# Kernel tuning notes

Hardware: AMD Instinct MI355X
Metric: run time of the kernel (lower is better)

## Reference

```python
import jax, jax.numpy as jnp
import numpy as np
import math

NUM_HEADS = 16
NUM_KV_HEADS = 4
HEAD_DIM = 128
ROPE_THETA = 10000.0


def _rope(x, cos, sin):
    # x: [b, h, s, d]; cos/sin: [1, 1, s, d//2]
    half = x.shape[-1] // 2
    x1, x2 = x[..., :half], x[..., half:]
    return jnp.concatenate([x1 * cos - x2 * sin, x2 * cos + x1 * sin], axis=-1)


def setup_inputs() -> dict:
    key = jax.random.key(0)
    ks = jax.random.split(key, 5)
    B, S, H = 2, 2048, 2048
    scale_qk = (2.0 / (H + H)) ** 0.5
    scale_kv = (2.0 / (H + NUM_KV_HEADS * HEAD_DIM)) ** 0.5
    return {
        "hidden_states": jax.random.normal(ks[0], (B, S, H), jnp.float32),
        "Wq": jax.random.normal(ks[1], (NUM_HEADS * HEAD_DIM, H), jnp.float32) * scale_qk,
        "Wk": jax.random.normal(ks[2], (NUM_KV_HEADS * HEAD_DIM, H), jnp.float32) * scale_kv,
        "Wv": jax.random.normal(ks[3], (NUM_KV_HEADS * HEAD_DIM, H), jnp.float32) * scale_kv,
        "Wo": jax.random.normal(ks[4], (NUM_HEADS * HEAD_DIM, H), jnp.float32) * scale_qk,
    }


def reference(hidden_states, Wq, Wk, Wv, Wo):
    B, S, H = hidden_states.shape
    hd = HEAD_DIM

    q = (hidden_states @ Wq.T).reshape(B, S, NUM_HEADS, hd).transpose(0, 2, 1, 3)
    k = (hidden_states @ Wk.T).reshape(B, S, NUM_KV_HEADS, hd).transpose(0, 2, 1, 3)
    v = (hidden_states @ Wv.T).reshape(B, S, NUM_KV_HEADS, hd).transpose(0, 2, 1, 3)

    # RoPE (half-split variant, as in module)
    inv_freq = 1.0 / (ROPE_THETA ** (jnp.arange(0, hd, 2, dtype=jnp.float32) / hd))
    pos = jnp.arange(S, dtype=jnp.float32)
    freqs = pos[:, None] * inv_freq[None, :]           # [S, hd//2]
    cos = jnp.cos(freqs)[None, None]                   # [1,1,S,hd//2]
    sin = jnp.sin(freqs)[None, None]
    q = _rope(q, cos, sin)
    k = _rope(k, cos, sin)

    # GQA: repeat kv heads (repeat_interleave semantics)
    n_rep = NUM_HEADS // NUM_KV_HEADS
    k = jnp.repeat(k, n_rep, axis=1)
    v = jnp.repeat(v, n_rep, axis=1)

    scores = jnp.einsum("bhqd,bhkd->bhqk", q, k) / math.sqrt(hd)
    attn = jax.nn.softmax(scores, axis=-1)
    out = jnp.einsum("bhqk,bhkd->bhqd", attn, v)
    out = out.transpose(0, 2, 1, 3).reshape(B, S, NUM_HEADS * hd)
    return out @ Wo.T
```

## Files before the change

### kernel.cpp

```cpp
#include <hip/hip_runtime.h>
#include <cstdint>
#include <cstddef>

typedef __bf16 bf16x8 __attribute__((ext_vector_type(8)));
typedef __bf16 bf16x4 __attribute__((ext_vector_type(4)));
typedef float  f32x4  __attribute__((ext_vector_type(4)));

__device__ __forceinline__ void gload_lds16(const void* g, void* l) {
    __builtin_amdgcn_global_load_lds(
        (const __attribute__((address_space(1))) void*)g,
        (__attribute__((address_space(3))) void*)l, 16, 0, 0);
}

#define VM6B asm volatile("s_waitcnt vmcnt(6) lgkmcnt(0)\ns_barrier" ::: "memory")
#define VM4B asm volatile("s_waitcnt vmcnt(4) lgkmcnt(0)\ns_barrier" ::: "memory")
#define VM0B asm volatile("s_waitcnt vmcnt(0) lgkmcnt(0)\ns_barrier" ::: "memory")
#define BARO asm volatile("s_barrier" ::: "memory")
#define WAITB4 asm volatile("s_waitcnt vmcnt(4) lgkmcnt(0)\ns_barrier" ::: "memory")
#define WAITB0 asm volatile("s_waitcnt vmcnt(0) lgkmcnt(0)\ns_barrier" ::: "memory")

#define SEQ 2048
#define NH 16
#define NKV 4
#define HD 128

__global__ __launch_bounds__(256) void cvt_all(const float* __restrict__ hs,
                                               const float* __restrict__ wq,
                                               const float* __restrict__ wk,
                                               const float* __restrict__ wv,
                                               const float* __restrict__ wo,
                                               __bf16* __restrict__ hB,
                                               __bf16* __restrict__ WqkB,
                                               __bf16* __restrict__ WvB,
                                               __bf16* __restrict__ WoB) {
    for (int bid = blockIdx.x; bid < 18432; bid += gridDim.x) {
        const float* in; __bf16* out; int base;
        if (bid < 8192)        { in = hs; out = hB;                   base = bid; }
        else if (bid < 12288)  { in = wq; out = WqkB;                 base = bid - 8192; }
        else if (bid < 13312)  { in = wk; out = WqkB + 2048 * 2048;   base = bid - 12288; }
        else if (bid < 14336)  { in = wv; out = WvB;                  base = bid - 13312; }
        else                   { in = wo; out = WoB;                  base = bid - 14336; }
        int i = base * 256 + threadIdx.x;
        float4 v = ((const float4*)in)[i];
        bf16x4 o = { (__bf16)v.x, (__bf16)v.y, (__bf16)v.z, (__bf16)v.w };
        ((bf16x4*)out)[i] = o;
    }
}

__device__ __forceinline__ void stage_half(const __bf16* __restrict__ M,
                                           char* dbuf, int bmn, int k0, int half,
                                           int wave, int lane) {
    char* hb = dbuf + (half & 1) * 32768 + (half >> 1) * 16384;
    int kbase = k0 + (half >> 1) * 32;
#pragma unroll
    for (int g = 0; g < 2; ++g) {
        int c = wave * 2 + g;
        int row = (c & 3) * 64 + lane;
        int ks = c >> 2;
        gload_lds16(M + (size_t)(bmn + row) * 2048 + kbase + ks * 8, hb + c * 1024);
    }
}

template <int KS, int MH>
__device__ __forceinline__ void phase_mfma(const __bf16* bA, const __bf16* bB,
                                           int quad, int l16, int wr128, int colbase,
                                           bf16x8 (&bq)[4], f32x4 acc[8][4]) {
    bf16x8 af[4];
#pragma unroll
    for (int ii = 0; ii < 4; ++ii)
        af[ii] = *(const bf16x8*)(bA + (KS * 4 + quad) * 2048 +
                                  (wr128 + (MH * 4 + ii) * 16 + l16) * 8);
    if (MH == 0) {
#pragma unroll
        for (int j = 0; j < 4; ++j)
            bq[j] = *(const bf16x8*)(bB + (KS * 4 + quad) * 2048 +
                                     (colbase + (j & 1) * 16 + (j >> 1) * 64 + l16) * 8);
    }
    __builtin_amdgcn_s_setprio(1);
#pragma unroll
    for (int ii = 0; ii < 4; ++ii)
#pragma unroll
        for (int j = 0; j < 4; ++j)
            acc[MH * 4 + ii][j] = __builtin_amdgcn_mfma_f32_16x16x32_bf16(
                af[ii], bq[j], acc[MH * 4 + ii][j], 0, 0, 0);
    __builtin_amdgcn_s_setprio(0);
}

__device__ __forceinline__ void gemm_core(const __bf16* __restrict__ A,
                                          const __bf16* __restrict__ B,
                                          char* lds, int bm, int bn,
                                          int wave, int lane, int quad, int l16,
                                          int wr128, int colbase, f32x4 acc[8][4]) {
    const int NT = 32;
    stage_half(A, lds, bm, 0, 0, wave, lane);
    stage_half(B, lds, bn, 0, 1, wave, lane);
    stage_half(A, lds, bm, 0, 2, wave, lane);
    stage_half(B, lds, bn, 0, 3, wave, lane);
    int cur = 0;
    for (int t = 0; t < NT - 1; ++t) {
        const __bf16* bA = (const __bf16*)(lds + cur * 65536);
        const __bf16* bB = (const __bf16*)(lds + cur * 65536 + 32768);
        char* nb = lds + (cur ^ 1) * 65536;
        int k1 = (t + 1) * 64;
        bf16x8 bq[4];
        stage_half(A, nb, bm, k1, 0, wave, lane);
        VM6B;
        phase_mfma<0, 0>(bA, bB, quad, l16, wr128, colbase, bq, acc);
        stage_half(B, nb, bn, k1, 1, wave, lane);
        BARO;
        phase_mfma<0, 1>(bA, bB, quad, l16, wr128, colbase, bq, acc);
        stage_half(A, nb, bm, k1, 2, wave, lane);
        VM6B;
        phase_mfma<1, 0>(bA, bB, quad, l16, wr128, colbase, bq, acc);
        stage_half(B, nb, bn, k1, 3, wave, lane);
        BARO;
        phase_mfma<1, 1>(bA, bB, quad, l16, wr128, colbase, bq, acc);
        cur ^= 1;
    }
    {
        const __bf16* bA = (const __bf16*)(lds + cur * 65536);
        const __bf16* bB = (const __bf16*)(lds + cur * 65536 + 32768);
        bf16x8 bq[4];
        VM4B;
        phase_mfma<0, 0>(bA, bB, quad, l16, wr128, colbase, bq, acc);
        phase_mfma<0, 1>(bA, bB, quad, l16, wr128, colbase, bq, acc);
        VM0B;
        phase_mfma<1, 0>(bA, bB, quad, l16, wr128, colbase, bq, acc);
        phase_mfma<1, 1>(bA, bB, quad, l16, wr128, colbase, bq, acc);
    }
}

__global__ __launch_bounds__(512, 2) void qkv_gemm(const __bf16* __restrict__ hB,
                                                   const __bf16* __restrict__ Wqk,
                                                   const __bf16* __restrict__ Wv,
                                                   __bf16* __restrict__ Qr,
                                                   __bf16* __restrict__ Kr,
                                                   __bf16* __restrict__ VT) {
    __shared__ __align__(16) char lds[2 * 65536];
    const int tid = threadIdx.x;
    const int wave = tid >> 6, lane = tid & 63;
    const int quad = lane >> 4, l16 = lane & 15;
    const int wr = wave >> 2, wc = wave & 3;
    int wg = blockIdx.y * 16 + blockIdx.x;
    wg = (wg & 7) * 24 + (wg >> 3);
    const int x = wg & 15, y = wg >> 4;
    const bool isVT = (y >= 10);
    const bool isQ = (y < 8);

    const __bf16* Amat = isVT ? Wv : hB;
    const __bf16* Bmat = isVT ? hB : (isQ ? Wqk : Wqk + 2048 * 2048);
    const int bm = isVT ? (y - 10) * 256 : x * 256;
    const int bn = isVT ? x * 256 : (isQ ? y * 256 : (y - 8) * 256);

    const int wr128 = wr * 128;
    const int colbase = (wc >> 1) * 128 + (wc & 1) * 32;

    f32x4 acc[8][4] = {};
    gemm_core(Amat, Bmat, lds, bm, bn, wave, lane, quad, l16, wr128, colbase, acc);

    if (isVT) {
#pragma unroll
        for (int i = 0; i < 8; ++i)
#pragma unroll
            for (int j = 0; j < 4; ++j) {
                int row = bm + wr128 + i * 16 + quad * 4;
                int col = bn + colbase + (j & 1) * 16 + (j >> 1) * 64 + l16;
#pragma unroll
                for (int r = 0; r < 4; ++r)
                    VT[(size_t)(row + r) * 4096 + col] = (__bf16)acc[i][j][r];
            }
    } else {
        __bf16* outp = isQ ? Qr : Kr;
        const float sc = isQ ? 0.1275255128608411f : 1.0f;
        const int nh = isQ ? NH : NKV;
        const int hh = (isQ ? y * 2 : (y - 8) * 2) + (wc >> 1);
#pragma unroll
        for (int j2 = 0; j2 < 2; ++j2) {
            int d = (wc & 1) * 32 + j2 * 16 + l16;
            float inv = exp2f(-(float)d * 0.2076205059304601f);
#pragma unroll
            for (int i = 0; i < 8; ++i)
#pragma unroll
                for (int r = 0; r < 4; ++r) {
                    int m = bm + wr128 + i * 16 + quad * 4 + r;
                    int s = m & (SEQ - 1), b = m >> 11;
                    float f = (float)s * inv;
                    float c = __cosf(f) * sc, sn = __sinf(f) * sc;
                    float x1 = acc[i][j2][r], x2 = acc[i][j2 + 2][r];
                    size_t rb = ((size_t)(b * nh + hh) * SEQ + s) * HD;
                    outp[rb + d]      = (__bf16)(x1 * c - x2 * sn);
                    outp[rb + d + 64] = (__bf16)(x2 * c + x1 * sn);
                }
        }
    }
}

__global__ __launch_bounds__(512, 1) void gemm_bt_f32(const __bf16* __restrict__ A,
                                                      const __bf16* __restrict__ W,
                                                      float* __restrict__ C) {
    __shared__ __align__(16) char lds[3 * 49152];
    const int tid = threadIdx.x;
    const int wave = tid >> 6, lane = tid & 63;
    const int quad = lane >> 4, l16 = lane & 15;
    const int wr = wave >> 2, wc = wave & 3;
    int wg = blockIdx.y * 32 + blockIdx.x;
    wg = (wg & 7) * 32 + (wg >> 3);
    const int bm = (wg & 31) * 128, bn = (wg >> 5) * 256;

    f32x4 acc[4][4] = {};

    auto stageT = [&](int sb, int k0) {
        char* dst = lds + sb * 49152;
#pragma unroll
        for (int tt = 0; tt < 6; ++tt) {
            int c = wave * 6 + tt;
            if (c < 16) {
                int row = ((c & 1) << 6) + lane;
                gload_lds16(A + (size_t)(bm + row) * 2048 + k0 + (c >> 1) * 8,
                            dst + c * 1024);
            } else {
                int vc = c - 16;
                int row = ((vc & 3) << 6) + lane;
                gload_lds16(W + (size_t)(bn + row) * 2048 + k0 + (vc >> 2) * 8,
                            dst + 16384 + vc * 1024);
            }
        }
    };

    auto computeT = [&](int cb2) {
        const __bf16* bA = (const __bf16*)(lds + cb2 * 49152);
        const __bf16* bB = bA + 8192;
#pragma unroll
        for (int ks = 0; ks < 2; ++ks) {
            bf16x8 af[4], bq[4];
#pragma unroll
            for (int i = 0; i < 4; ++i)
                af[i] = *(const bf16x8*)(bA + (ks * 4 + quad) * 1024 +
                                         (wr * 64 + i * 16 + l16) * 8);
#pragma unroll
            for (int j = 0; j < 4; ++j)
                bq[j] = *(const bf16x8*)(bB + (ks * 4 + quad) * 2048 +
                                         (wc * 64 + j * 16 + l16) * 8);
            __builtin_amdgcn_s_setprio(1);
#pragma unroll
            for (int i = 0; i < 4; ++i)
#pragma unroll
                for (int j = 0; j < 4; ++j)
                    acc[i][j] = __builtin_amdgcn_mfma_f32_16x16x32_bf16(
                        af[i], bq[j], acc[i][j], 0, 0, 0);
            __builtin_amdgcn_s_setprio(0);
        }
    };

    stageT(0, 0);
    stageT(1, 64);
    int cb = 0;
    for (int t = 0; t < 31; ++t) {
        VM6B;
        if (t < 30) {
            int sb = cb + 2; if (sb >= 3) sb -= 3;
            stageT(sb, (t + 2) * 64);
        }
        computeT(cb);
        if (++cb == 3) cb = 0;
    }
    VM0B;
    computeT(cb);

#pragma unroll
    for (int i = 0; i < 4; ++i)
#pragma unroll
        for (int j = 0; j < 4; ++j) {
            int row = bm + wr * 64 + i * 16 + quad * 4;
            int col = bn + wc * 64 + j * 16 + l16;
#pragma unroll
            for (int r = 0; r < 4; ++r)
                C[(size_t)(row + r) * 2048 + col] = acc[i][j][r];
        }
}

__global__ __launch_bounds__(256, 2) void attn_kernel(const __bf16* __restrict__ Q,
                                                      const __bf16* __restrict__ Kr,
                                                      const __bf16* __restrict__ VT,
                                                      __bf16* __restrict__ AO) {
    __shared__ __align__(16) char ring[3 * 16384];
    __shared__ __align__(16) __bf16 Pb[4][32][40];

    const int tid = threadIdx.x;
    const int wave = tid >> 6, lane = tid & 63;
    const int quad = lane >> 4, l16 = lane & 15;
    int wg = (blockIdx.z * 16 + blockIdx.y) * 16 + blockIdx.x;
    wg = (wg & 7) * 64 + (wg >> 3);
    const int x = wg & 15, h = (wg >> 4) & 15, b = wg >> 8;
    const int kv = h >> 2;
    const int qbase = x * 128 + wave * 32;

    bf16x8 qf[2][4];
#pragma unroll
    for (int qs = 0; qs < 2; ++qs) {
        const __bf16* Qp =
            Q + ((size_t)(b * NH + h) * SEQ + qbase + qs * 16 + l16) * HD + quad * 8;
#pragma unroll
        for (int kq = 0; kq < 4; ++kq) qf[qs][kq] = *(const bf16x8*)(Qp + kq * 32);
    }

    const __bf16* Kp = Kr + (size_t)(b * NKV + kv) * SEQ * HD;
    const __bf16* Vp = VT + (size_t)(kv * HD) * (2 * SEQ) + b * SEQ;

    f32x4 oacc[2][8] = {};
    float lpart[2] = {0.f, 0.f};

    auto stage = [&](int sb, int k0) {
        char* dst = ring + sb * 16384;
#pragma unroll
        for (int tt = 0; tt < 4; ++tt) {
            int c = wave * 4 + tt;
            if (c < 8) {
                gload_lds16(Kp + (size_t)(k0 + (lane & 31)) * HD +
                                (2 * c + (lane >> 5)) * 8,
                            dst + c * 1024);
            } else {
                int vc = c - 8;
                gload_lds16(Vp + (size_t)(((vc & 1) << 6) + lane) * (2 * SEQ) + k0 +
                                (vc >> 1) * 8,
                            dst + 8192 + vc * 1024);
            }
        }
    };

    auto compute = [&](int cb) {
        const __bf16* kt = (const __bf16*)(ring + cb * 16384);
        const __bf16* vt = kt + 4096;
#pragma unroll
        for (int mt = 0; mt < 2; ++mt) {
            f32x4 s0 = {0.f, 0.f, 0.f, 0.f}, s1 = {0.f, 0.f, 0.f, 0.f};
#pragma unroll
            for (int kq = 0; kq < 4; ++kq) {
                bf16x8 ka = *(const bf16x8*)(kt + (kq * 4 + quad) * 256 +
                                             (mt * 16 + l16) * 8);
                s0 = __builtin_amdgcn_mfma_f32_16x16x32_bf16(ka, qf[0][kq], s0, 0, 0, 0);
                s1 = __builtin_amdgcn_mfma_f32_16x16x32_bf16(ka, qf[1][kq], s1, 0, 0, 0);
            }
            bf16x4 pk0, pk1;
#pragma unroll
            for (int r = 0; r < 4; ++r) {
                float p0 = __builtin_amdgcn_exp2f(s0[r]);
                float p1 = __builtin_amdgcn_exp2f(s1[r]);
                lpart[0] += p0; lpart[1] += p1;
                pk0[r] = (__bf16)p0; pk1[r] = (__bf16)p1;
            }
            *(bf16x4*)&Pb[wave][l16][mt * 16 + quad * 4] = pk0;
            *(bf16x4*)&Pb[wave][16 + l16][mt * 16 + quad * 4] = pk1;
        }
        bf16x8 pb0 = *(const bf16x8*)&Pb[wave][l16][quad * 8];
        bf16x8 pb1 = *(const bf16x8*)&Pb[wave][16 + l16][quad * 8];
#pragma unroll
        for (int mt = 0; mt < 8; ++mt) {
            bf16x8 va = *(const bf16x8*)(vt + quad * 1024 + (mt * 16 + l16) * 8);
            oacc[0][mt] = __builtin_amdgcn_mfma_f32_16x16x32_bf16(
                va, pb0, oacc[0][mt], 0, 0, 0);
            oacc[1][mt] = __builtin_amdgcn_mfma_f32_16x16x32_bf16(
                va, pb1, oacc[1][mt], 0, 0, 0);
        }
    };

    stage(0, 0);
    stage(1, 32);
    int cb = 0;
    for (int t = 0; t < 63; ++t) {
        WAITB4;
        if (t < 62) {
            int sb = cb + 2; if (sb >= 3) sb -= 3;
            stage(sb, (t + 2) * 32);
        }
        compute(cb);
        if (++cb == 3) cb = 0;
    }
    WAITB0;
    compute(cb);

#pragma unroll
    for (int qs = 0; qs < 2; ++qs) {
        lpart[qs] += __shfl_xor(lpart[qs], 16);
        lpart[qs] += __shfl_xor(lpart[qs], 32);
        float inv = 1.f / lpart[qs];
        int q = qbase + qs * 16 + l16;
#pragma unroll
        for (int mt = 0; mt < 8; ++mt) {
            bf16x4 ov;
#pragma unroll
            for (int r = 0; r < 4; ++r) ov[r] = (__bf16)(oacc[qs][mt][r] * inv);
            *(bf16x4*)(AO + ((size_t)(b * SEQ + q)) * (NH * HD) + h * HD +
                       mt * 16 + quad * 4) = ov;
        }
    }
}

extern "C" void kernel_launch(void* const* d_in, const int* in_sizes, int n_in,
                              void* d_out, int out_size, void* d_ws, size_t ws_size,
                              hipStream_t stream) {
    const float* hs = (const float*)d_in[0];
    const float* Wq = (const float*)d_in[1];
    const float* Wk = (const float*)d_in[2];
    const float* Wv = (const float*)d_in[3];
    const float* Wo = (const float*)d_in[4];
    float* out = (float*)d_out;
    char* ws = (char*)d_ws;

    __bf16* Qr   = (__bf16*)(ws + 0);
    __bf16* Kr   = (__bf16*)(ws + 16777216);
    __bf16* VT   = (__bf16*)(ws + 20971520);
    __bf16* WoB  = (__bf16*)(ws + 25165824);
    __bf16* hB   = (__bf16*)(ws + 33554432);
    __bf16* WqkB = (__bf16*)(ws + 50331648);
    __bf16* WvB  = (__bf16*)(ws + 60817408);
    __bf16* AO   = (__bf16*)(ws + 33554432);

    cvt_all<<<2048, 256, 0, stream>>>(hs, Wq, Wk, Wv, Wo, hB, WqkB, WvB, WoB);

    qkv_gemm<<<dim3(16, 12), 512, 0, stream>>>(hB, WqkB, WvB, Qr, Kr, VT);

    attn_kernel<<<dim3(16, 16, 2), 256, 0, stream>>>(Qr, Kr, VT, AO);

    gemm_bt_f32<<<dim3(32, 8), 512, 0, stream>>>(AO, WoB, out);
}
```

Baseline: 332.7 us.

## Fuse all four stages into one cooperative persistent kernel with grid syncs

Replaces the four separate launches (conversion, QKV GEMM, attention, output GEMM) with a single cooperative kernel of 256 blocks that runs each stage as a phase separated by grid.sync. The Wo conversion is moved off the critical path into the idle blocks during the QKV GEMM phase. The aim is to remove launch gaps and the tail of each kernel. In exchange, occupancy is pinned to one 512-thread block per CU. Attention now runs two 256-thread groups per block instead of two independent blocks, which may reduce latency hiding, and grid syncs add their own cost.

```diff
diff --git a/kernel.cpp b/kernel.cpp
--- a/kernel.cpp
+++ b/kernel.cpp
@@ -1,6 +1,9 @@
 #include <hip/hip_runtime.h>
+#include <hip/hip_cooperative_groups.h>
 #include <cstdint>
 #include <cstddef>
+
+namespace cg = cooperative_groups;
 
 typedef __bf16 bf16x8 __attribute__((ext_vector_type(8)));
 typedef __bf16 bf16x4 __attribute__((ext_vector_type(4)));
@@ -23,29 +26,6 @@
 #define NH 16
 #define NKV 4
 #define HD 128
-
-__global__ __launch_bounds__(256) void cvt_all(const float* __restrict__ hs,
-                                               const float* __restrict__ wq,
-                                               const float* __restrict__ wk,
-                                               const float* __restrict__ wv,
-                                               const float* __restrict__ wo,
-                                               __bf16* __restrict__ hB,
-                                               __bf16* __restrict__ WqkB,
-                                               __bf16* __restrict__ WvB,
-                                               __bf16* __restrict__ WoB) {
-    for (int bid = blockIdx.x; bid < 18432; bid += gridDim.x) {
-        const float* in; __bf16* out; int base;
-        if (bid < 8192)        { in = hs; out = hB;                   base = bid; }
-        else if (bid < 12288)  { in = wq; out = WqkB;                 base = bid - 8192; }
-        else if (bid < 13312)  { in = wk; out = WqkB + 2048 * 2048;   base = bid - 12288; }
-        else if (bid < 14336)  { in = wv; out = WvB;                  base = bid - 13312; }
-        else                   { in = wo; out = WoB;                  base = bid - 14336; }
-        int i = base * 256 + threadIdx.x;
-        float4 v = ((const float4*)in)[i];
-        bf16x4 o = { (__bf16)v.x, (__bf16)v.y, (__bf16)v.z, (__bf16)v.w };
-        ((bf16x4*)out)[i] = o;
-    }
-}
 
 __device__ __forceinline__ void stage_half(const __bf16* __restrict__ M,
                                            char* dbuf, int bmn, int k0, int half,
@@ -130,19 +110,18 @@
     }
 }
 
-__global__ __launch_bounds__(512, 2) void qkv_gemm(const __bf16* __restrict__ hB,
-                                                   const __bf16* __restrict__ Wqk,
-                                                   const __bf16* __restrict__ Wv,
-                                                   __bf16* __restrict__ Qr,
-                                                   __bf16* __restrict__ Kr,
-                                                   __bf16* __restrict__ VT) {
-    __shared__ __align__(16) char lds[2 * 65536];
+__device__ __forceinline__ void qkv_phase(char* lds, int wg0,
+                                          const __bf16* __restrict__ hB,
+                                          const __bf16* __restrict__ Wqk,
+                                          const __bf16* __restrict__ Wv,
+                                          __bf16* __restrict__ Qr,
+                                          __bf16* __restrict__ Kr,
+                                          __bf16* __restrict__ VT) {
     const int tid = threadIdx.x;
     const int wave = tid >> 6, lane = tid & 63;
     const int quad = lane >> 4, l16 = lane & 15;
     const int wr = wave >> 2, wc = wave & 3;
-    int wg = blockIdx.y * 16 + blockIdx.x;
-    wg = (wg & 7) * 24 + (wg >> 3);
+    int wg = (wg0 & 7) * 24 + (wg0 >> 3);
     const int x = wg & 15, y = wg >> 4;
     const bool isVT = (y >= 10);
     const bool isQ = (y < 8);
@@ -195,16 +174,129 @@
     }
 }
 
-__global__ __launch_bounds__(512, 1) void gemm_bt_f32(const __bf16* __restrict__ A,
-                                                      const __bf16* __restrict__ W,
-                                                      float* __restrict__ C) {
-    __shared__ __align__(16) char lds[3 * 49152];
+__device__ __forceinline__ void attn_phase(char* ring, __bf16 (*Pb)[32][40], int v,
+                                           const __bf16* __restrict__ Q,
+                                           const __bf16* __restrict__ Kr,
+                                           const __bf16* __restrict__ VT,
+                                           __bf16* __restrict__ AO) {
+    const int tid = threadIdx.x;
+    const int wave = (tid >> 6) & 3, lane = tid & 63;
+    const int quad = lane >> 4, l16 = lane & 15;
+    int wg = (v & 7) * 64 + (v >> 3);
+    const int x = wg & 15, h = (wg >> 4) & 15, b = wg >> 8;
+    const int kv = h >> 2;
+    const int qbase = x * 128 + wave * 32;
+
+    bf16x8 qf[2][4];
+#pragma unroll
+    for (int qs = 0; qs < 2; ++qs) {
+        const __bf16* Qp =
+            Q + ((size_t)(b * NH + h) * SEQ + qbase + qs * 16 + l16) * HD + quad * 8;
+#pragma unroll
+        for (int kq = 0; kq < 4; ++kq) qf[qs][kq] = *(const bf16x8*)(Qp + kq * 32);
+    }
+
+    const __bf16* Kp = Kr + (size_t)(b * NKV + kv) * SEQ * HD;
+    const __bf16* Vp = VT + (size_t)(kv * HD) * (2 * SEQ) + b * SEQ;
+
+    f32x4 oacc[2][8] = {};
+    float lpart[2] = {0.f, 0.f};
+
+    auto stage = [&](int sb, int k0) {
+        char* dst = ring + sb * 16384;
+#pragma unroll
+        for (int tt = 0; tt < 4; ++tt) {
+            int c = wave * 4 + tt;
+            if (c < 8) {
+                gload_lds16(Kp + (size_t)(k0 + (lane & 31)) * HD +
+                                (2 * c + (lane >> 5)) * 8,
+                            dst + c * 1024);
+            } else {
+                int vc = c - 8;
+                gload_lds16(Vp + (size_t)(((vc & 1) << 6) + lane) * (2 * SEQ) + k0 +
+                                (vc >> 1) * 8,
+                            dst + 8192 + vc * 1024);
+            }
+        }
+    };
+
+    auto compute = [&](int cb) {
+        const __bf16* kt = (const __bf16*)(ring + cb * 16384);
+        const __bf16* vt = kt + 4096;
+#pragma unroll
+        for (int mt = 0; mt < 2; ++mt) {
+            f32x4 s0 = {0.f, 0.f, 0.f, 0.f}, s1 = {0.f, 0.f, 0.f, 0.f};
+#pragma unroll
+            for (int kq = 0; kq < 4; ++kq) {
+                bf16x8 ka = *(const bf16x8*)(kt + (kq * 4 + quad) * 256 +
+                                             (mt * 16 + l16) * 8);
+                s0 = __builtin_amdgcn_mfma_f32_16x16x32_bf16(ka, qf[0][kq], s0, 0, 0, 0);
+                s1 = __builtin_amdgcn_mfma_f32_16x16x32_bf16(ka, qf[1][kq], s1, 0, 0, 0);
+            }
+            bf16x4 pk0, pk1;
+#pragma unroll
+            for (int r = 0; r < 4; ++r) {
+                float p0 = __builtin_amdgcn_exp2f(s0[r]);
+                float p1 = __builtin_amdgcn_exp2f(s1[r]);
+                lpart[0] += p0; lpart[1] += p1;
+                pk0[r] = (__bf16)p0; pk1[r] = (__bf16)p1;
+            }
+            *(bf16x4*)&Pb[wave][l16][mt * 16 + quad * 4] = pk0;
+            *(bf16x4*)&Pb[wave][16 + l16][mt * 16 + quad * 4] = pk1;
+        }
+        bf16x8 pb0 = *(const bf16x8*)&Pb[wave][l16][quad * 8];
+        bf16x8 pb1 = *(const bf16x8*)&Pb[wave][16 + l16][quad * 8];
+#pragma unroll
+        for (int mt = 0; mt < 8; ++mt) {
+            bf16x8 va = *(const bf16x8*)(vt + quad * 1024 + (mt * 16 + l16) * 8);
+            oacc[0][mt] = __builtin_amdgcn_mfma_f32_16x16x32_bf16(
+                va, pb0, oacc[0][mt], 0, 0, 0);
+            oacc[1][mt] = __builtin_amdgcn_mfma_f32_16x16x32_bf16(
+                va, pb1, oacc[1][mt], 0, 0, 0);
+        }
+    };
+
+    stage(0, 0);
+    stage(1, 32);
+    int cb = 0;
+    for (int t = 0; t < 63; ++t) {
+        WAITB4;
+        if (t < 62) {
+            int sb = cb + 2; if (sb >= 3) sb -= 3;
+            stage(sb, (t + 2) * 32);
+        }
+        compute(cb);
+        if (++cb == 3) cb = 0;
+    }
+    WAITB0;
+    compute(cb);
+
+#pragma unroll
+    for (int qs = 0; qs < 2; ++qs) {
+        lpart[qs] += __shfl_xor(lpart[qs], 16);
+        lpart[qs] += __shfl_xor(lpart[qs], 32);
+        float inv = 1.f / lpart[qs];
+        int q = qbase + qs * 16 + l16;
+#pragma unroll
+        for (int mt = 0; mt < 8; ++mt) {
+            bf16x4 ov;
+#pragma unroll
+            for (int r = 0; r < 4; ++r) ov[r] = (__bf16)(oacc[qs][mt][r] * inv);
+            *(bf16x4*)(AO + ((size_t)(b * SEQ + q)) * (NH * HD) + h * HD +
+                       mt * 16 + quad * 4) = ov;
+        }
+    }
+}
+
+__device__ __forceinline__ void bt_phase(char* lds, int wg0,
+                                         const __bf16* __restrict__ A,
+                                         const __bf16* __restrict__ W,
+                                         float* __restrict__ C) {
     const int tid = threadIdx.x;
     const int wave = tid >> 6, lane = tid & 63;
     const int quad = lane >> 4, l16 = lane & 15;
     const int wr = wave >> 2, wc = wave & 3;
-    int wg = blockIdx.y * 32 + blockIdx.x;
-    wg = (wg & 7) * 32 + (wg >> 3);
+    int wg = (wg0 & 7) * 32 + (wg0 >> 3);
     const int bm = (wg & 31) * 128, bn = (wg >> 5) * 256;
 
     f32x4 acc[4][4] = {};
@@ -279,121 +371,64 @@
         }
 }
 
-__global__ __launch_bounds__(256, 2) void attn_kernel(const __bf16* __restrict__ Q,
-                                                      const __bf16* __restrict__ Kr,
-                                                      const __bf16* __restrict__ VT,
-                                                      __bf16* __restrict__ AO) {
-    __shared__ __align__(16) char ring[3 * 16384];
-    __shared__ __align__(16) __bf16 Pb[4][32][40];
-
+__global__ __launch_bounds__(512, 1) void mega(const float* __restrict__ hs,
+                                               const float* __restrict__ wq,
+                                               const float* __restrict__ wk,
+                                               const float* __restrict__ wv,
+                                               const float* __restrict__ wo,
+                                               __bf16* __restrict__ hB,
+                                               __bf16* __restrict__ WqkB,
+                                               __bf16* __restrict__ WvB,
+                                               __bf16* __restrict__ WoB,
+                                               __bf16* __restrict__ Qr,
+                                               __bf16* __restrict__ Kr,
+                                               __bf16* __restrict__ VT,
+                                               __bf16* __restrict__ AO,
+                                               float* __restrict__ out) {
+    __shared__ __align__(16) char smem[147456];
+    cg::grid_group grid = cg::this_grid();
     const int tid = threadIdx.x;
-    const int wave = tid >> 6, lane = tid & 63;
-    const int quad = lane >> 4, l16 = lane & 15;
-    int wg = (blockIdx.z * 16 + blockIdx.y) * 16 + blockIdx.x;
-    wg = (wg & 7) * 64 + (wg >> 3);
-    const int x = wg & 15, h = (wg >> 4) & 15, b = wg >> 8;
-    const int kv = h >> 2;
-    const int qbase = x * 128 + wave * 32;
-
-    bf16x8 qf[2][4];
-#pragma unroll
-    for (int qs = 0; qs < 2; ++qs) {
-        const __bf16* Qp =
-            Q + ((size_t)(b * NH + h) * SEQ + qbase + qs * 16 + l16) * HD + quad * 8;
-#pragma unroll
-        for (int kq = 0; kq < 4; ++kq) qf[qs][kq] = *(const bf16x8*)(Qp + kq * 32);
-    }
-
-    const __bf16* Kp = Kr + (size_t)(b * NKV + kv) * SEQ * HD;
-    const __bf16* Vp = VT + (size_t)(kv * HD) * (2 * SEQ) + b * SEQ;
-
-    f32x4 oacc[2][8] = {};
-    float lpart[2] = {0.f, 0.f};
-
-    auto stage = [&](int sb, int k0) {
-        char* dst = ring + sb * 16384;
-#pragma unroll
-        for (int tt = 0; tt < 4; ++tt) {
-            int c = wave * 4 + tt;
-            if (c < 8) {
-                gload_lds16(Kp + (size_t)(k0 + (lane & 31)) * HD +
-                                (2 * c + (lane >> 5)) * 8,
-                            dst + c * 1024);
-            } else {
-                int vc = c - 8;
-                gload_lds16(Vp + (size_t)(((vc & 1) << 6) + lane) * (2 * SEQ) + k0 +
-                                (vc >> 1) * 8,
-                            dst + 8192 + vc * 1024);
-            }
-        }
-    };
-
-    auto compute = [&](int cb) {
-        const __bf16* kt = (const __bf16*)(ring + cb * 16384);
-        const __bf16* vt = kt + 4096;
-#pragma unroll
-        for (int mt = 0; mt < 2; ++mt) {
-            f32x4 s0 = {0.f, 0.f, 0.f, 0.f}, s1 = {0.f, 0.f, 0.f, 0.f};
-#pragma unroll
-            for (int kq = 0; kq < 4; ++kq) {
-                bf16x8 ka = *(const bf16x8*)(kt + (kq * 4 + quad) * 256 +
-                                             (mt * 16 + l16) * 8);
-                s0 = __builtin_amdgcn_mfma_f32_16x16x32_bf16(ka, qf[0][kq], s0, 0, 0, 0);
-                s1 = __builtin_amdgcn_mfma_f32_16x16x32_bf16(ka, qf[1][kq], s1, 0, 0, 0);
-            }
-            bf16x4 pk0, pk1;
-#pragma unroll
-            for (int r = 0; r < 4; ++r) {
-                float p0 = __builtin_amdgcn_exp2f(s0[r]);
-                float p1 = __builtin_amdgcn_exp2f(s1[r]);
-                lpart[0] += p0; lpart[1] += p1;
-                pk0[r] = (__bf16)p0; pk1[r] = (__bf16)p1;
-            }
-            *(bf16x4*)&Pb[wave][l16][mt * 16 + quad * 4] = pk0;
-            *(bf16x4*)&Pb[wave][16 + l16][mt * 16 + quad * 4] = pk1;
-        }
-        bf16x8 pb0 = *(const bf16x8*)&Pb[wave][l16][quad * 8];
-        bf16x8 pb1 = *(const bf16x8*)&Pb[wave][16 + l16][quad * 8];
-#pragma unroll
-        for (int mt = 0; mt < 8; ++mt) {
-            bf16x8 va = *(const bf16x8*)(vt + quad * 1024 + (mt * 16 + l16) * 8);
-            oacc[0][mt] = __builtin_amdgcn_mfma_f32_16x16x32_bf16(
-                va, pb0, oacc[0][mt], 0, 0, 0);
-            oacc[1][mt] = __builtin_amdgcn_mfma_f32_16x16x32_bf16(
-                va, pb1, oacc[1][mt], 0, 0, 0);
-        }
-    };
-
-    stage(0, 0);
-    stage(1, 32);
-    int cb = 0;
-    for (int t = 0; t < 63; ++t) {
-        WAITB4;
-        if (t < 62) {
-            int sb = cb + 2; if (sb >= 3) sb -= 3;
-            stage(sb, (t + 2) * 32);
-        }
-        compute(cb);
-        if (++cb == 3) cb = 0;
-    }
-    WAITB0;
-    compute(cb);
-
-#pragma unroll
-    for (int qs = 0; qs < 2; ++qs) {
-        lpart[qs] += __shfl_xor(lpart[qs], 16);
-        lpart[qs] += __shfl_xor(lpart[qs], 32);
-        float inv = 1.f / lpart[qs];
-        int q = qbase + qs * 16 + l16;
-#pragma unroll
-        for (int mt = 0; mt < 8; ++mt) {
-            bf16x4 ov;
-#pragma unroll
-            for (int r = 0; r < 4; ++r) ov[r] = (__bf16)(oacc[qs][mt][r] * inv);
-            *(bf16x4*)(AO + ((size_t)(b * SEQ + q)) * (NH * HD) + h * HD +
-                       mt * 16 + quad * 4) = ov;
-        }
-    }
+    const int rb = blockIdx.x;
+
+    {
+        int half = tid >> 8, t256 = tid & 255;
+        for (int it = 0; it < 28; ++it) {
+            int vb = it * 512 + rb * 2 + half;
+            const float* in; __bf16* outp; int base;
+            if (vb < 8192)       { in = hs; outp = hB;               base = vb; }
+            else if (vb < 12288) { in = wq; outp = WqkB;             base = vb - 8192; }
+            else if (vb < 13312) { in = wk; outp = WqkB + 2048*2048; base = vb - 12288; }
+            else                 { in = wv; outp = WvB;              base = vb - 13312; }
+            int i = base * 256 + t256;
+            float4 v = ((const float4*)in)[i];
+            bf16x4 o = { (__bf16)v.x, (__bf16)v.y, (__bf16)v.z, (__bf16)v.w };
+            ((bf16x4*)outp)[i] = o;
+        }
+    }
+    grid.sync();
+
+    if (rb < 192) {
+        qkv_phase(smem, rb, hB, WqkB, WvB, Qr, Kr, VT);
+    } else {
+        int bbase = rb - 192;
+        for (int it = 0; it < 32; ++it) {
+            int idx = (it * 64 + bbase) * 512 + tid;
+            float4 v = ((const float4*)wo)[idx];
+            bf16x4 o = { (__bf16)v.x, (__bf16)v.y, (__bf16)v.z, (__bf16)v.w };
+            ((bf16x4*)WoB)[idx] = o;
+        }
+    }
+    grid.sync();
+
+    {
+        int g = tid >> 8;
+        char* ring = smem + g * 49152;
+        __bf16 (*Pb)[32][40] = (__bf16(*)[32][40])(smem + 98304 + g * 10240);
+        attn_phase(ring, Pb, rb * 2 + g, Qr, Kr, VT, AO);
+    }
+    grid.sync();
+
+    bt_phase(smem, rb, AO, WoB, out);
 }
 
 extern "C" void kernel_launch(void* const* d_in, const int* in_sizes, int n_in,
@@ -416,11 +451,9 @@
     __bf16* WvB  = (__bf16*)(ws + 60817408);
     __bf16* AO   = (__bf16*)(ws + 33554432);
 
-    cvt_all<<<2048, 256, 0, stream>>>(hs, Wq, Wk, Wv, Wo, hB, WqkB, WvB, WoB);
-
-    qkv_gemm<<<dim3(16, 12), 512, 0, stream>>>(hB, WqkB, WvB, Qr, Kr, VT);
-
-    attn_kernel<<<dim3(16, 16, 2), 256, 0, stream>>>(Qr, Kr, VT, AO);
-
-    gemm_bt_f32<<<dim3(32, 8), 512, 0, stream>>>(AO, WoB, out);
-}
+    void* kargs[] = { (void*)&hs, (void*)&Wq, (void*)&Wk, (void*)&Wv, (void*)&Wo,
+                      (void*)&hB, (void*)&WqkB, (void*)&WvB, (void*)&WoB,
+                      (void*)&Qr, (void*)&Kr, (void*)&VT, (void*)&AO, (void*)&out };
+    hipLaunchCooperativeKernel((const void*)mega, dim3(256), dim3(512),
+                               kargs, 0, stream);
+}
```

After: 459.1 us. 38.0% more time.
